# Kernel tuning notes

Measured on AMD Instinct MI355X. Metric: run time of the kernel, lower is better.

Reference implementation:

```python
import jax, jax.numpy as jnp
import numpy as np


def setup_inputs() -> dict:
    key = jax.random.key(0)
    k1, k2, k3, k4, k5 = jax.random.split(key, 5)
    B, S, E2, D = 32, 2048, 1024, 512
    return {
        "output_encoder": jax.random.normal(k1, (B, S, E2), dtype=jnp.float32),
        "last_hidden_decoder": jax.random.normal(k2, (B, D), dtype=jnp.float32),
        "W_att": jax.random.normal(k3, (E2 + D, D), dtype=jnp.float32) * 0.02,
        "b_att": jax.random.normal(k4, (D,), dtype=jnp.float32) * 0.02,
        "v": jax.random.normal(k5, (D,), dtype=jnp.float32) * 0.02,
    }


def reference(output_encoder, last_hidden_decoder, W_att, b_att, v):
    # output_encoder: (B, S, E2); last_hidden_decoder: (B, D)
    B, S, E2 = output_encoder.shape
    D = last_hidden_decoder.shape[-1]
    # Split W_att to avoid materializing the repeated+concat tensor:
    # concat(enc, dec) @ W == enc @ W_enc + dec @ W_dec  (dec broadcast over seq)
    W_enc, W_dec = W_att[:E2], W_att[E2:]
    dec_proj = last_hidden_decoder @ W_dec  # (B, D)
    energy = jnp.tanh(jnp.einsum("bse,ed->bsd", output_encoder, W_enc)
                      + dec_proj[:, None, :] + b_att)  # (B, S, D)
    attention = jnp.einsum("bsd,d->bs", energy, v)  # (B, S)
    attention_weights = jax.nn.softmax(attention, axis=1)  # (B, S)
    # context: (B, 1, E2)
    context = jnp.einsum("bs,bse->be", attention_weights, output_encoder)[:, None, :]
    return context
```

## Files before the change

### kernel.cpp

```cpp
#include <hip/hip_runtime.h>
#include <stdint.h>


typedef __attribute__((ext_vector_type(8))) __bf16 bf16x8;
typedef __attribute__((ext_vector_type(4))) float f32x4;

__device__ __forceinline__ uint16_t f32_to_bf16_rne(float f) {
  union { float f; uint32_t u; } v; v.f = f;
  uint32_t u = v.u;
  return (uint16_t)((u + 0x7FFFu + ((u >> 16) & 1u)) >> 16);
}

__device__ __forceinline__ float tanh_fast(float x) {
  float e = __expf(2.0f * x);
  return 1.0f - 2.0f * __builtin_amdgcn_rcpf(e + 1.0f);
}

__global__ __launch_bounds__(256) void prep_kernel(
    const float* __restrict__ dec,
    const float* __restrict__ Watt,
    const float* __restrict__ batt,
    float* __restrict__ cbias,
    uint16_t* __restrict__ Wb,
    float* __restrict__ out)
{
  const int t = blockIdx.x * 256 + threadIdx.x;

  for (int i = t; i < 32768; i += 16384) out[i] = 0.0f;

  {
    const int b = t >> 9, d = t & 511;
    const float* wd = Watt + 1024 * 512 + d;
    const float* dv = dec + b * 512;
    float s0 = 0.f, s1 = 0.f, s2 = 0.f, s3 = 0.f;
    #pragma unroll 4
    for (int k = 0; k < 512; k += 4) {
      s0 += dv[k + 0] * wd[(k + 0) * 512];
      s1 += dv[k + 1] * wd[(k + 1) * 512];
      s2 += dv[k + 2] * wd[(k + 2) * 512];
      s3 += dv[k + 3] * wd[(k + 3) * 512];
    }
    cbias[t] = batt[d] + ((s0 + s1) + (s2 + s3));
  }

  uint4* WbV = (uint4*)Wb;
  #pragma unroll
  for (int i = 0; i < 4; ++i) {
    const int u   = t + 16384 * i;
    const int c   = u >> 11;
    const int rem = u & 2047;
    const int wn  = rem >> 8;
    const int nf  = (rem >> 6) & 3;
    const int ln  = rem & 63;
    const int kb  = c * 32 + ((ln >> 4) << 3);
    const int d   = wn * 64 + nf * 16 + (ln & 15);
    uint32_t h[8];
    #pragma unroll
    for (int kk = 0; kk < 8; ++kk) {
      float f = Watt[(size_t)(kb + kk) * 512 + d];
      h[kk] = f32_to_bf16_rne(f);
    }
    uint4 val;
    val.x = h[0] | (h[1] << 16);
    val.y = h[2] | (h[3] << 16);
    val.z = h[4] | (h[5] << 16);
    val.w = h[6] | (h[7] << 16);
    WbV[u] = val;
  }
}

__global__ __launch_bounds__(512, 4) void energy_kernel(
    const float* __restrict__ x,
    const uint16_t* __restrict__ Wb,
    const float* __restrict__ cbias,
    const float* __restrict__ vvec,
    float* __restrict__ att)
{
  __shared__ __align__(16) uint8_t AL[2][64 * 64];

  const int tid  = threadIdx.x;
  const int lane = tid & 63;
  const int wave = tid >> 6;
  const int l15  = lane & 15;
  const int l4   = lane >> 4;
  const int brow0 = blockIdx.x * 64;
  const int b     = brow0 >> 11;

  const int r_st = tid >> 3, q_st = tid & 7;
  const int aoff = r_st * 64 + ((q_st * 8) ^ (((r_st >> 1) & 3) << 4));
  const float* asrc = x + (size_t)(brow0 + r_st) * 1024 + q_st * 4;
  const uint8_t* wslice = (const uint8_t*)Wb + (size_t)wave * 4096 + (size_t)lane * 16;

  f32x4 acc[4][4];
  #pragma unroll
  for (int mf = 0; mf < 4; ++mf)
    #pragma unroll
    for (int nf = 0; nf < 4; ++nf)
      acc[mf][nf] = (f32x4){0.f, 0.f, 0.f, 0.f};

  float4 av_cur = *(const float4*)(asrc);
  bf16x8 bA[4], bB[4];
  {
    const bf16x8* bs = (const bf16x8*)(wslice);
    bA[0] = bs[0]; bA[1] = bs[64]; bA[2] = bs[128]; bA[3] = bs[192];
  }

#define CHUNK(C, BCUR, BNXT)                                                   \
  {                                                                            \
    const int c_ = (C);                                                        \
    uint8_t* Ab = AL[c_ & 1];                                                  \
    uint32_t lo_ = (uint32_t)f32_to_bf16_rne(av_cur.x) |                       \
                   ((uint32_t)f32_to_bf16_rne(av_cur.y) << 16);                \
    uint32_t hi_ = (uint32_t)f32_to_bf16_rne(av_cur.z) |                       \
                   ((uint32_t)f32_to_bf16_rne(av_cur.w) << 16);                \
    *(uint2*)(Ab + aoff) = make_uint2(lo_, hi_);                               \
    const int cn_ = (c_ < 31) ? c_ + 1 : 31;                                   \
    av_cur = *(const float4*)(asrc + cn_ * 32);                                \
    asm volatile("s_waitcnt lgkmcnt(0)" ::: "memory");                         \
    __builtin_amdgcn_s_barrier();                                              \
    asm volatile("" ::: "memory");                                             \
    {                                                                          \
      const bf16x8* bs_ = (const bf16x8*)(wslice + (size_t)cn_ * 32768);       \
      BNXT[0] = bs_[0]; BNXT[1] = bs_[64];                                     \
      BNXT[2] = bs_[128]; BNXT[3] = bs_[192];                                  \
    }                                                                          \
    _Pragma("unroll")                                                          \
    for (int mf = 0; mf < 4; ++mf) {                                           \
      const int r_ = mf * 16 + l15;                                            \
      bf16x8 afm = *(const bf16x8*)(Ab + r_ * 64 +                             \
                                    ((l4 * 16) ^ (((r_ >> 1) & 3) << 4)));     \
      acc[mf][0] = __builtin_amdgcn_mfma_f32_16x16x32_bf16(afm, BCUR[0], acc[mf][0], 0, 0, 0); \
      acc[mf][1] = __builtin_amdgcn_mfma_f32_16x16x32_bf16(afm, BCUR[1], acc[mf][1], 0, 0, 0); \
      acc[mf][2] = __builtin_amdgcn_mfma_f32_16x16x32_bf16(afm, BCUR[2], acc[mf][2], 0, 0, 0); \
      acc[mf][3] = __builtin_amdgcn_mfma_f32_16x16x32_bf16(afm, BCUR[3], acc[mf][3], 0, 0, 0); \
    }                                                                          \
  }

  for (int c = 0; c < 32; c += 2) {
    CHUNK(c, bA, bB);
    CHUNK(c + 1, bB, bA);
  }
#undef CHUNK

  float cb[4], vv[4];
  #pragma unroll
  for (int nf = 0; nf < 4; ++nf) {
    const int d = wave * 64 + nf * 16 + l15;
    cb[nf] = cbias[b * 512 + d];
    vv[nf] = vvec[d];
  }

  __syncthreads();
  float* red = (float*)AL;
  if (tid < 64) red[tid] = 0.0f;
  __syncthreads();

  #pragma unroll
  for (int mf = 0; mf < 4; ++mf) {
    float s[4] = {0.f, 0.f, 0.f, 0.f};
    #pragma unroll
    for (int nf = 0; nf < 4; ++nf) {
      #pragma unroll
      for (int j = 0; j < 4; ++j) {
        const float e = acc[mf][nf][j] + cb[nf];
        s[j] += tanh_fast(e) * vv[nf];
      }
    }
    #pragma unroll
    for (int j = 0; j < 4; ++j) {
      float r = s[j];
      r += __shfl_xor(r, 1);
      r += __shfl_xor(r, 2);
      r += __shfl_xor(r, 4);
      r += __shfl_xor(r, 8);
      if (l15 == 0) atomicAdd(&red[mf * 16 + 4 * l4 + j], r);
    }
  }
  __syncthreads();
  if (tid < 64) att[brow0 + tid] = red[tid];
}

__global__ __launch_bounds__(256) void softmax_kernel(float* __restrict__ att) {
  const int b = blockIdx.x;
  float* row = att + b * 2048;
  const int tid = threadIdx.x;
  __shared__ float redm[4], reds[4];

  float vals[8];
  float m = -1e30f;
  #pragma unroll
  for (int i = 0; i < 8; ++i) { vals[i] = row[tid + 256 * i]; m = fmaxf(m, vals[i]); }
  #pragma unroll
  for (int msk = 1; msk < 64; msk <<= 1) m = fmaxf(m, __shfl_xor(m, msk));
  if ((tid & 63) == 0) redm[tid >> 6] = m;
  __syncthreads();
  m = fmaxf(fmaxf(redm[0], redm[1]), fmaxf(redm[2], redm[3]));

  float s = 0.f;
  #pragma unroll
  for (int i = 0; i < 8; ++i) { vals[i] = __expf(vals[i] - m); s += vals[i]; }
  #pragma unroll
  for (int msk = 1; msk < 64; msk <<= 1) s += __shfl_xor(s, msk);
  if ((tid & 63) == 0) reds[tid >> 6] = s;
  __syncthreads();
  const float inv = 1.0f / (((reds[0] + reds[1]) + (reds[2] + reds[3])));
  #pragma unroll
  for (int i = 0; i < 8; ++i) row[tid + 256 * i] = vals[i] * inv;
}

__global__ __launch_bounds__(256) void context_kernel(
    const float* __restrict__ x,
    const float* __restrict__ w,
    float* __restrict__ out)
{
  const int blk = blockIdx.x;
  const int b = blk >> 4, sc = blk & 15;
  const int tid = threadIdx.x;
  const float* xb = x + ((size_t)(b * 2048 + sc * 128)) * 1024 + tid * 4;
  const float* wb = w + b * 2048 + sc * 128;

  float4 acc = {0.f, 0.f, 0.f, 0.f};
  for (int si = 0; si < 128; ++si) {
    const float ww = wb[si];
    const float4 xv = *(const float4*)(xb + (size_t)si * 1024);
    acc.x += ww * xv.x;
    acc.y += ww * xv.y;
    acc.z += ww * xv.z;
    acc.w += ww * xv.w;
  }
  float* o = out + b * 1024 + tid * 4;
  atomicAdd(o + 0, acc.x);
  atomicAdd(o + 1, acc.y);
  atomicAdd(o + 2, acc.z);
  atomicAdd(o + 3, acc.w);
}

extern "C" void kernel_launch(void* const* d_in, const int* in_sizes, int n_in,
                              void* d_out, int out_size, void* d_ws, size_t ws_size,
                              hipStream_t stream) {
  const float* x    = (const float*)d_in[0];
  const float* dec  = (const float*)d_in[1];
  const float* Watt = (const float*)d_in[2];
  const float* batt = (const float*)d_in[3];
  const float* v    = (const float*)d_in[4];
  float* out = (float*)d_out;

  uint8_t* ws = (uint8_t*)d_ws;
  float*    att   = (float*)ws;
  float*    cbias = (float*)(ws + 256 * 1024);
  uint16_t* Wb    = (uint16_t*)(ws + 320 * 1024);

  prep_kernel<<<64, 256, 0, stream>>>(dec, Watt, batt, cbias, Wb, out);
  energy_kernel<<<1024, 512, 0, stream>>>(x, Wb, cbias, v, att);
  softmax_kernel<<<32, 256, 0, stream>>>(att);
  context_kernel<<<512, 256, 0, stream>>>(x, att, out);
}
```

Baseline: 143.8 us.

## Widen energy GEMM K-chunk to 64 and split context kernel finer

```diff
diff --git a/kernel.cpp b/kernel.cpp
--- a/kernel.cpp
+++ b/kernel.cpp
@@ -76,7 +76,7 @@
     const float* __restrict__ vvec,
     float* __restrict__ att)
 {
-  __shared__ __align__(16) uint8_t AL[2][64 * 64];
+  __shared__ __align__(16) uint8_t AL[2][64 * 128];
 
   const int tid  = threadIdx.x;
   const int lane = tid & 63;
@@ -87,7 +87,8 @@
   const int b     = brow0 >> 11;
 
   const int r_st = tid >> 3, q_st = tid & 7;
-  const int aoff = r_st * 64 + ((q_st * 8) ^ (((r_st >> 1) & 3) << 4));
+  const int aoff0 = r_st * 128 + ((q_st * 8) ^ ((r_st & 7) << 4));
+  const int aoff1 = r_st * 128 + (((q_st + 8) * 8) ^ ((r_st & 7) << 4));
   const float* asrc = x + (size_t)(brow0 + r_st) * 1024 + q_st * 4;
   const uint8_t* wslice = (const uint8_t*)Wb + (size_t)wave * 4096 + (size_t)lane * 16;
 
@@ -98,49 +99,51 @@
     for (int nf = 0; nf < 4; ++nf)
       acc[mf][nf] = (f32x4){0.f, 0.f, 0.f, 0.f};
 
-  float4 av_cur = *(const float4*)(asrc);
-  bf16x8 bA[4], bB[4];
-  {
-    const bf16x8* bs = (const bf16x8*)(wslice);
-    bA[0] = bs[0]; bA[1] = bs[64]; bA[2] = bs[128]; bA[3] = bs[192];
-  }
-
-#define CHUNK(C, BCUR, BNXT)                                                   \
-  {                                                                            \
-    const int c_ = (C);                                                        \
-    uint8_t* Ab = AL[c_ & 1];                                                  \
-    uint32_t lo_ = (uint32_t)f32_to_bf16_rne(av_cur.x) |                       \
-                   ((uint32_t)f32_to_bf16_rne(av_cur.y) << 16);                \
-    uint32_t hi_ = (uint32_t)f32_to_bf16_rne(av_cur.z) |                       \
-                   ((uint32_t)f32_to_bf16_rne(av_cur.w) << 16);                \
-    *(uint2*)(Ab + aoff) = make_uint2(lo_, hi_);                               \
-    const int cn_ = (c_ < 31) ? c_ + 1 : 31;                                   \
-    av_cur = *(const float4*)(asrc + cn_ * 32);                                \
-    asm volatile("s_waitcnt lgkmcnt(0)" ::: "memory");                         \
-    __builtin_amdgcn_s_barrier();                                              \
-    asm volatile("" ::: "memory");                                             \
-    {                                                                          \
-      const bf16x8* bs_ = (const bf16x8*)(wslice + (size_t)cn_ * 32768);       \
-      BNXT[0] = bs_[0]; BNXT[1] = bs_[64];                                     \
-      BNXT[2] = bs_[128]; BNXT[3] = bs_[192];                                  \
-    }                                                                          \
-    _Pragma("unroll")                                                          \
-    for (int mf = 0; mf < 4; ++mf) {                                           \
-      const int r_ = mf * 16 + l15;                                            \
-      bf16x8 afm = *(const bf16x8*)(Ab + r_ * 64 +                             \
-                                    ((l4 * 16) ^ (((r_ >> 1) & 3) << 4)));     \
-      acc[mf][0] = __builtin_amdgcn_mfma_f32_16x16x32_bf16(afm, BCUR[0], acc[mf][0], 0, 0, 0); \
-      acc[mf][1] = __builtin_amdgcn_mfma_f32_16x16x32_bf16(afm, BCUR[1], acc[mf][1], 0, 0, 0); \
-      acc[mf][2] = __builtin_amdgcn_mfma_f32_16x16x32_bf16(afm, BCUR[2], acc[mf][2], 0, 0, 0); \
-      acc[mf][3] = __builtin_amdgcn_mfma_f32_16x16x32_bf16(afm, BCUR[3], acc[mf][3], 0, 0, 0); \
-    }                                                                          \
-  }
-
-  for (int c = 0; c < 32; c += 2) {
-    CHUNK(c, bA, bB);
-    CHUNK(c + 1, bB, bA);
-  }
-#undef CHUNK
+  float4 av0 = *(const float4*)(asrc);
+  float4 av1 = *(const float4*)(asrc + 32);
+
+  for (int i = 0; i < 16; ++i) {
+    uint8_t* Ab = AL[i & 1];
+
+    {
+      uint32_t lo = (uint32_t)f32_to_bf16_rne(av0.x) | ((uint32_t)f32_to_bf16_rne(av0.y) << 16);
+      uint32_t hi = (uint32_t)f32_to_bf16_rne(av0.z) | ((uint32_t)f32_to_bf16_rne(av0.w) << 16);
+      *(uint2*)(Ab + aoff0) = make_uint2(lo, hi);
+      lo = (uint32_t)f32_to_bf16_rne(av1.x) | ((uint32_t)f32_to_bf16_rne(av1.y) << 16);
+      hi = (uint32_t)f32_to_bf16_rne(av1.z) | ((uint32_t)f32_to_bf16_rne(av1.w) << 16);
+      *(uint2*)(Ab + aoff1) = make_uint2(lo, hi);
+    }
+    if (i < 15) {
+      av0 = *(const float4*)(asrc + (i + 1) * 64);
+      av1 = *(const float4*)(asrc + (i + 1) * 64 + 32);
+    }
+    asm volatile("s_waitcnt lgkmcnt(0)" ::: "memory");
+    __builtin_amdgcn_s_barrier();
+    asm volatile("" ::: "memory");
+
+    const bf16x8* bs = (const bf16x8*)(wslice + (size_t)i * 65536);
+    bf16x8 b0 = bs[0],    b1 = bs[64],     b2 = bs[128],     b3 = bs[192];
+    bf16x8 b4 = bs[2048], b5 = bs[2048+64], b6 = bs[2048+128], b7 = bs[2048+192];
+
+    #pragma unroll
+    for (int mf = 0; mf < 4; ++mf) {
+      const int r = mf * 16 + l15;
+      bf16x8 afm = *(const bf16x8*)(Ab + r * 128 + ((l4 * 16) ^ ((r & 7) << 4)));
+      acc[mf][0] = __builtin_amdgcn_mfma_f32_16x16x32_bf16(afm, b0, acc[mf][0], 0, 0, 0);
+      acc[mf][1] = __builtin_amdgcn_mfma_f32_16x16x32_bf16(afm, b1, acc[mf][1], 0, 0, 0);
+      acc[mf][2] = __builtin_amdgcn_mfma_f32_16x16x32_bf16(afm, b2, acc[mf][2], 0, 0, 0);
+      acc[mf][3] = __builtin_amdgcn_mfma_f32_16x16x32_bf16(afm, b3, acc[mf][3], 0, 0, 0);
+    }
+    #pragma unroll
+    for (int mf = 0; mf < 4; ++mf) {
+      const int r = mf * 16 + l15;
+      bf16x8 afm = *(const bf16x8*)(Ab + r * 128 + (((64 + l4 * 16)) ^ ((r & 7) << 4)));
+      acc[mf][0] = __builtin_amdgcn_mfma_f32_16x16x32_bf16(afm, b4, acc[mf][0], 0, 0, 0);
+      acc[mf][1] = __builtin_amdgcn_mfma_f32_16x16x32_bf16(afm, b5, acc[mf][1], 0, 0, 0);
+      acc[mf][2] = __builtin_amdgcn_mfma_f32_16x16x32_bf16(afm, b6, acc[mf][2], 0, 0, 0);
+      acc[mf][3] = __builtin_amdgcn_mfma_f32_16x16x32_bf16(afm, b7, acc[mf][3], 0, 0, 0);
+    }
+  }
 
   float cb[4], vv[4];
   #pragma unroll
@@ -214,13 +217,14 @@
     float* __restrict__ out)
 {
   const int blk = blockIdx.x;
-  const int b = blk >> 4, sc = blk & 15;
+  const int b = blk >> 6, sc = blk & 63;
   const int tid = threadIdx.x;
-  const float* xb = x + ((size_t)(b * 2048 + sc * 128)) * 1024 + tid * 4;
-  const float* wb = w + b * 2048 + sc * 128;
+  const float* xb = x + ((size_t)(b * 2048 + sc * 32)) * 1024 + tid * 4;
+  const float* wb = w + b * 2048 + sc * 32;
 
   float4 acc = {0.f, 0.f, 0.f, 0.f};
-  for (int si = 0; si < 128; ++si) {
+  #pragma unroll 4
+  for (int si = 0; si < 32; ++si) {
     const float ww = wb[si];
     const float4 xv = *(const float4*)(xb + (size_t)si * 1024);
     acc.x += ww * xv.x;
@@ -253,5 +257,5 @@
   prep_kernel<<<64, 256, 0, stream>>>(dec, Watt, batt, cbias, Wb, out);
   energy_kernel<<<1024, 512, 0, stream>>>(x, Wb, cbias, v, att);
   softmax_kernel<<<32, 256, 0, stream>>>(att);
-  context_kernel<<<512, 256, 0, stream>>>(x, att, out);
-}
+  context_kernel<<<2048, 256, 0, stream>>>(x, att, out);
+}
```

After: 156.6 us. +8.9%, slower.

## Load A fragments directly from global per wave, dropping LDS staging and barriers

Applied to the files above, without the earlier changes.

```diff
diff --git a/kernel.cpp b/kernel.cpp
--- a/kernel.cpp
+++ b/kernel.cpp
@@ -9,6 +9,21 @@
   union { float f; uint32_t u; } v; v.f = f;
   uint32_t u = v.u;
   return (uint16_t)((u + 0x7FFFu + ((u >> 16) & 1u)) >> 16);
+}
+
+__device__ __forceinline__ uint32_t cvtpk_bf16(float lo, float hi) {
+  uint32_t r;
+  asm("v_cvt_pk_bf16_f32 %0, %1, %2" : "=v"(r) : "v"(lo), "v"(hi));
+  return r;
+}
+
+__device__ __forceinline__ bf16x8 cvt8(f32x4 lo, f32x4 hi) {
+  union { uint32_t w[4]; bf16x8 v; } u;
+  u.w[0] = cvtpk_bf16(lo.x, lo.y);
+  u.w[1] = cvtpk_bf16(lo.z, lo.w);
+  u.w[2] = cvtpk_bf16(hi.x, hi.y);
+  u.w[3] = cvtpk_bf16(hi.z, hi.w);
+  return u.v;
 }
 
 __device__ __forceinline__ float tanh_fast(float x) {
@@ -76,7 +91,7 @@
     const float* __restrict__ vvec,
     float* __restrict__ att)
 {
-  __shared__ __align__(16) uint8_t AL[2][64 * 64];
+  __shared__ float red[64];
 
   const int tid  = threadIdx.x;
   const int lane = tid & 63;
@@ -86,9 +101,7 @@
   const int brow0 = blockIdx.x * 64;
   const int b     = brow0 >> 11;
 
-  const int r_st = tid >> 3, q_st = tid & 7;
-  const int aoff = r_st * 64 + ((q_st * 8) ^ (((r_st >> 1) & 3) << 4));
-  const float* asrc = x + (size_t)(brow0 + r_st) * 1024 + q_st * 4;
+  const float* arow0 = x + (size_t)(brow0 + l15) * 1024 + l4 * 8;
   const uint8_t* wslice = (const uint8_t*)Wb + (size_t)wave * 4096 + (size_t)lane * 16;
 
   f32x4 acc[4][4];
@@ -98,7 +111,6 @@
     for (int nf = 0; nf < 4; ++nf)
       acc[mf][nf] = (f32x4){0.f, 0.f, 0.f, 0.f};
 
-  float4 av_cur = *(const float4*)(asrc);
   bf16x8 bA[4], bB[4];
   {
     const bf16x8* bs = (const bf16x8*)(wslice);
@@ -107,28 +119,19 @@
 
 #define CHUNK(C, BCUR, BNXT)                                                   \
   {                                                                            \
-    const int c_ = (C);                                                        \
-    uint8_t* Ab = AL[c_ & 1];                                                  \
-    uint32_t lo_ = (uint32_t)f32_to_bf16_rne(av_cur.x) |                       \
-                   ((uint32_t)f32_to_bf16_rne(av_cur.y) << 16);                \
-    uint32_t hi_ = (uint32_t)f32_to_bf16_rne(av_cur.z) |                       \
-                   ((uint32_t)f32_to_bf16_rne(av_cur.w) << 16);                \
-    *(uint2*)(Ab + aoff) = make_uint2(lo_, hi_);                               \
-    const int cn_ = (c_ < 31) ? c_ + 1 : 31;                                   \
-    av_cur = *(const float4*)(asrc + cn_ * 32);                                \
-    asm volatile("s_waitcnt lgkmcnt(0)" ::: "memory");                         \
-    __builtin_amdgcn_s_barrier();                                              \
-    asm volatile("" ::: "memory");                                             \
+    const int c_  = (C);                                                       \
+    const int cn_ = (c_ + 1 < 32) ? c_ + 1 : 31;                               \
     {                                                                          \
       const bf16x8* bs_ = (const bf16x8*)(wslice + (size_t)cn_ * 32768);       \
-      BNXT[0] = bs_[0]; BNXT[1] = bs_[64];                                     \
+      BNXT[0] = bs_[0];  BNXT[1] = bs_[64];                                    \
       BNXT[2] = bs_[128]; BNXT[3] = bs_[192];                                  \
     }                                                                          \
     _Pragma("unroll")                                                          \
     for (int mf = 0; mf < 4; ++mf) {                                           \
-      const int r_ = mf * 16 + l15;                                            \
-      bf16x8 afm = *(const bf16x8*)(Ab + r_ * 64 +                             \
-                                    ((l4 * 16) ^ (((r_ >> 1) & 3) << 4)));     \
+      const float* ap = arow0 + (size_t)mf * 16384 + c_ * 32;                  \
+      f32x4 lo = *(const f32x4*)(ap);                                          \
+      f32x4 hi = *(const f32x4*)(ap + 4);                                      \
+      bf16x8 afm = cvt8(lo, hi);                                               \
       acc[mf][0] = __builtin_amdgcn_mfma_f32_16x16x32_bf16(afm, BCUR[0], acc[mf][0], 0, 0, 0); \
       acc[mf][1] = __builtin_amdgcn_mfma_f32_16x16x32_bf16(afm, BCUR[1], acc[mf][1], 0, 0, 0); \
       acc[mf][2] = __builtin_amdgcn_mfma_f32_16x16x32_bf16(afm, BCUR[2], acc[mf][2], 0, 0, 0); \
@@ -150,8 +153,6 @@
     vv[nf] = vvec[d];
   }
 
-  __syncthreads();
-  float* red = (float*)AL;
   if (tid < 64) red[tid] = 0.0f;
   __syncthreads();
 
```

New measurement: 332.2 us. 2.31x slower.

## Stage four K-chunks per barrier with deeper A prefetch and MFMA priority

Applied to the files above, without the earlier changes.

```diff
diff --git a/kernel.cpp b/kernel.cpp
--- a/kernel.cpp
+++ b/kernel.cpp
@@ -76,7 +76,7 @@
     const float* __restrict__ vvec,
     float* __restrict__ att)
 {
-  __shared__ __align__(16) uint8_t AL[2][64 * 64];
+  __shared__ __align__(16) uint8_t AL[2][64 * 256];
 
   const int tid  = threadIdx.x;
   const int lane = tid & 63;
@@ -87,7 +87,10 @@
   const int b     = brow0 >> 11;
 
   const int r_st = tid >> 3, q_st = tid & 7;
-  const int aoff = r_st * 64 + ((q_st * 8) ^ (((r_st >> 1) & 3) << 4));
+  int aoffs[4];
+  #pragma unroll
+  for (int kc = 0; kc < 4; ++kc)
+    aoffs[kc] = r_st * 256 + ((kc * 64 + q_st * 8) ^ ((r_st & 7) << 4));
   const float* asrc = x + (size_t)(brow0 + r_st) * 1024 + q_st * 4;
   const uint8_t* wslice = (const uint8_t*)Wb + (size_t)wave * 4096 + (size_t)lane * 16;
 
@@ -98,49 +101,63 @@
     for (int nf = 0; nf < 4; ++nf)
       acc[mf][nf] = (f32x4){0.f, 0.f, 0.f, 0.f};
 
-  float4 av_cur = *(const float4*)(asrc);
+  f32x4 av[4];
+  #pragma unroll
+  for (int kc = 0; kc < 4; ++kc)
+    av[kc] = __builtin_nontemporal_load((const f32x4*)(asrc + kc * 32));
   bf16x8 bA[4], bB[4];
   {
     const bf16x8* bs = (const bf16x8*)(wslice);
     bA[0] = bs[0]; bA[1] = bs[64]; bA[2] = bs[128]; bA[3] = bs[192];
   }
 
-#define CHUNK(C, BCUR, BNXT)                                                   \
+#define DOCHUNK(I, KC, BCUR, BNXT)                                             \
   {                                                                            \
-    const int c_ = (C);                                                        \
-    uint8_t* Ab = AL[c_ & 1];                                                  \
-    uint32_t lo_ = (uint32_t)f32_to_bf16_rne(av_cur.x) |                       \
-                   ((uint32_t)f32_to_bf16_rne(av_cur.y) << 16);                \
-    uint32_t hi_ = (uint32_t)f32_to_bf16_rne(av_cur.z) |                       \
-                   ((uint32_t)f32_to_bf16_rne(av_cur.w) << 16);                \
-    *(uint2*)(Ab + aoff) = make_uint2(lo_, hi_);                               \
-    const int cn_ = (c_ < 31) ? c_ + 1 : 31;                                   \
-    av_cur = *(const float4*)(asrc + cn_ * 32);                                \
-    asm volatile("s_waitcnt lgkmcnt(0)" ::: "memory");                         \
-    __builtin_amdgcn_s_barrier();                                              \
-    asm volatile("" ::: "memory");                                             \
+    const int cg_ = 4 * (I) + (KC);                                            \
+    const int cn_ = (cg_ + 1 < 32) ? cg_ + 1 : 31;                             \
     {                                                                          \
       const bf16x8* bs_ = (const bf16x8*)(wslice + (size_t)cn_ * 32768);       \
-      BNXT[0] = bs_[0]; BNXT[1] = bs_[64];                                     \
+      BNXT[0] = bs_[0];   BNXT[1] = bs_[64];                                   \
       BNXT[2] = bs_[128]; BNXT[3] = bs_[192];                                  \
     }                                                                          \
     _Pragma("unroll")                                                          \
     for (int mf = 0; mf < 4; ++mf) {                                           \
       const int r_ = mf * 16 + l15;                                            \
-      bf16x8 afm = *(const bf16x8*)(Ab + r_ * 64 +                             \
-                                    ((l4 * 16) ^ (((r_ >> 1) & 3) << 4)));     \
+      bf16x8 afm = *(const bf16x8*)(Ab + r_ * 256 +                            \
+                    (((KC) * 64 + l4 * 16) ^ ((r_ & 7) << 4)));                \
+      __builtin_amdgcn_s_setprio(1);                                           \
       acc[mf][0] = __builtin_amdgcn_mfma_f32_16x16x32_bf16(afm, BCUR[0], acc[mf][0], 0, 0, 0); \
       acc[mf][1] = __builtin_amdgcn_mfma_f32_16x16x32_bf16(afm, BCUR[1], acc[mf][1], 0, 0, 0); \
       acc[mf][2] = __builtin_amdgcn_mfma_f32_16x16x32_bf16(afm, BCUR[2], acc[mf][2], 0, 0, 0); \
       acc[mf][3] = __builtin_amdgcn_mfma_f32_16x16x32_bf16(afm, BCUR[3], acc[mf][3], 0, 0, 0); \
+      __builtin_amdgcn_s_setprio(0);                                           \
     }                                                                          \
   }
 
-  for (int c = 0; c < 32; c += 2) {
-    CHUNK(c, bA, bB);
-    CHUNK(c + 1, bB, bA);
-  }
-#undef CHUNK
+  for (int i = 0; i < 8; ++i) {
+    uint8_t* Ab = AL[i & 1];
+
+    #pragma unroll
+    for (int kc = 0; kc < 4; ++kc) {
+      uint32_t lo = (uint32_t)f32_to_bf16_rne(av[kc].x) | ((uint32_t)f32_to_bf16_rne(av[kc].y) << 16);
+      uint32_t hi = (uint32_t)f32_to_bf16_rne(av[kc].z) | ((uint32_t)f32_to_bf16_rne(av[kc].w) << 16);
+      *(uint2*)(Ab + aoffs[kc]) = make_uint2(lo, hi);
+    }
+    if (i < 7) {
+      #pragma unroll
+      for (int kc = 0; kc < 4; ++kc)
+        av[kc] = __builtin_nontemporal_load((const f32x4*)(asrc + (i + 1) * 128 + kc * 32));
+    }
+    asm volatile("s_waitcnt lgkmcnt(0)" ::: "memory");
+    __builtin_amdgcn_s_barrier();
+    asm volatile("" ::: "memory");
+
+    DOCHUNK(i, 0, bA, bB);
+    DOCHUNK(i, 1, bB, bA);
+    DOCHUNK(i, 2, bA, bB);
+    DOCHUNK(i, 3, bB, bA);
+  }
+#undef DOCHUNK
 
   float cb[4], vv[4];
   #pragma unroll
```

After: 152.9 us. 6.4% more time.
